# Kernel optimization log

Hardware: AMD Instinct MI355X
Metric: run time of the kernel (lower is better)

## Reference

```python
import jax, jax.numpy as jnp
import numpy as np
import math

# Dims chosen per input_specs
B, Q, S, T = 8, 64, 64, 64          # batch, queries, stat (segment) count, tokens per segment
H, DH = 8, 64                        # heads, head dim
NH = H * DH                          # num_hiddens = 512
STAT_K, TOKEN_K = 8, 16
NEG = -1e6


def setup_inputs() -> dict:
    key = jax.random.key(0)
    ks = jax.random.split(key, 11)
    f = lambda k, sh: jax.random.normal(k, sh, dtype=jnp.float32)
    w = lambda k: f(k, (NH, NH)) * 0.05  # Linear weights stored as [in, out]
    return {
        "queries": f(ks[0], (B, Q, NH)),
        "stat_keys": f(ks[1], (B, S, NH)),
        "token_keys": f(ks[2], (B * S, T, NH)),
        "values": f(ks[3], (B * S, T, NH)),
        "stat_valid_lens": jax.random.randint(ks[4], (B,), 1, S + 1, dtype=jnp.int32),
        "Wq_stat": w(ks[5]),
        "Wq_token": w(ks[6]),
        "Wk_stat": w(ks[7]),
        "Wk_token": w(ks[8]),
        "Wv": w(ks[9]),
        "Wo": w(ks[10]),
    }


def reference(queries, stat_keys, token_keys, values, stat_valid_lens,
              Wq_stat, Wq_token, Wk_stat, Wk_token, Wv, Wo):
    scale = 1.0 / math.sqrt(DH)

    def split_heads(x):  # [b, L, H*DH] -> [b, H, L, DH]
        b, L, _ = x.shape
        return x.reshape(b, L, H, DH).transpose(0, 2, 1, 3)

    q_stat = split_heads(queries @ Wq_stat)        # [B,H,Q,DH]
    q_tok = split_heads(queries @ Wq_token)        # [B,H,Q,DH]
    k_stat = split_heads(stat_keys @ Wk_stat)      # [B,H,S,DH]
    # token_keys/values come in as [B*S, T, size]; per-head layout [B,H,S,T,DH]
    k_tok = (token_keys @ Wk_token).reshape(B, S, T, H, DH).transpose(0, 3, 1, 2, 4)
    v = (values @ Wv).reshape(B, S, T, H, DH).transpose(0, 3, 1, 2, 4)

    # --- stat-level scores, valid-length mask, top-k sparsification, softmax ---
    stat_scores = jnp.einsum('bhqd,bhsd->bhqs', q_stat, k_stat) * scale  # [B,H,Q,S]
    valid = jnp.arange(S)[None, None, None, :] < stat_valid_lens[:, None, None, None]
    stat_scores = jnp.where(valid, stat_scores, NEG)
    k1 = min(S - 1, STAT_K)
    _, top_idx = jax.lax.top_k(stat_scores, k1)                           # [B,H,Q,k1]
    keep = jax.nn.one_hot(top_idx, S, dtype=stat_scores.dtype).sum(-2) > 0  # [B,H,Q,S]
    stat_w = jax.nn.softmax(jnp.where(keep, stat_scores, NEG), axis=-1)   # [B,H,Q,S]

    # --- token-level scores. NOTE: the original code computes torch.topk but then
    # overwrites with the LAST k2 positions (token_weights[:, :, -k2:] = ...), so the
    # token top-k result is dead code; we faithfully reproduce the last-k2 masking. ---
    tok_scores = jnp.einsum('bhqd,bhstd->bhsqt', q_tok, k_tok) * scale    # [B,H,S,Q,T]
    k2 = min(T - 1, TOKEN_K)
    last_mask = jnp.arange(T) >= (T - k2)
    tok_w = jax.nn.softmax(jnp.where(last_mask, tok_scores, NEG), axis=-1)
    tok_w = tok_w.transpose(0, 1, 3, 2, 4)                                # [B,H,Q,S,T]

    # --- combine hierarchy and attend over values ---
    comb = stat_w[..., None] * tok_w                                      # [B,H,Q,S,T]
    out = jnp.einsum('bhqst,bhstd->bhqd', comb, v)                        # [B,H,Q,DH]
    out = out.transpose(0, 2, 1, 3).reshape(B, Q, NH)
    return out @ Wo
```

## Files before the change

### kernel.cpp

```cpp
#include <hip/hip_runtime.h>
#include <hip/hip_bf16.h>

#define STAT_K 8
#define TOKEN_K 16

typedef short bf16x8 __attribute__((ext_vector_type(8)));
typedef float f32x4 __attribute__((ext_vector_type(4)));

__device__ inline ushort f2bf_rne(float x) {
    union { float f; unsigned u; } v; v.f = x;
    unsigned r = v.u + 0x7fff + ((v.u >> 16) & 1);
    return (ushort)(r >> 16);
}
__device__ inline float bf2f(ushort h) {
    union { unsigned u; float f; } v; v.u = ((unsigned)h) << 16;
    return v.f;
}

__global__ __launch_bounds__(256) void conv_w(
    const float* w0, const float* w1, const float* w2,
    const float* w3, const float* w4, const float* w5,
    ushort* wT)
{
    const int z = blockIdx.z;
    const float* srcs[6] = {w0, w1, w2, w3, w4, w5};
    const float* src = srcs[z];
    ushort* hi = wT + (size_t)z * 524288;
    ushort* lo = hi + 262144;
    __shared__ float t[32][33];
    const int c0 = blockIdx.x * 32, r0 = blockIdx.y * 32;
    const int tx = threadIdx.x & 31, ty = threadIdx.x >> 5;
    #pragma unroll
    for (int i = 0; i < 4; ++i)
        t[ty + 8 * i][tx] = src[(r0 + ty + 8 * i) * 512 + c0 + tx];
    __syncthreads();
    #pragma unroll
    for (int i = 0; i < 4; ++i) {
        float x = t[tx][ty + 8 * i];
        ushort h = f2bf_rne(x);
        int o = (c0 + ty + 8 * i) * 512 + r0 + tx;
        hi[o] = h;
        lo[o] = f2bf_rne(x - bf2f(h));
    }
}

__global__ __launch_bounds__(256) void gemm_all(
    const float* __restrict__ queries, const float* __restrict__ stat_keys,
    const float* __restrict__ token_keys, const float* __restrict__ values,
    const ushort* __restrict__ wT,
    float* __restrict__ q_stat, float* __restrict__ k_stat,
    float* __restrict__ q_tokf,
    ushort* __restrict__ k_tok, ushort* __restrict__ v_projT)
{
    __shared__ ushort smem[12800];
    const int tid = threadIdx.x;
    const int bid = blockIdx.x;
    const int wave = tid >> 6, lane = tid & 63;
    const int m16 = lane & 15, quad = lane >> 4;
    const int srow = tid >> 2, schunk = tid & 3;

    if (bid < 192) {
        const int z = bid >> 6, t = bid & 63;
        const int row0 = (t >> 3) * 64, col0 = (t & 7) * 64;
        const float* A = (z == 1) ? stat_keys : queries;
        const ushort* Bh = wT + (size_t)z * 524288;
        const ushort* Bl = Bh + 262144;
        float* C = (z == 0) ? q_stat : (z == 1) ? k_stat : q_tokf;

        ushort* As_hi = smem;
        ushort* As_lo = smem + 2560;
        ushort* Bs_hi = smem + 5120;
        ushort* Bs_lo = smem + 7680;
        const int wm = wave & 1, wn = wave >> 1;

        f32x4 acc[2][2];
        #pragma unroll
        for (int i = 0; i < 2; ++i)
            #pragma unroll
            for (int j = 0; j < 2; ++j)
                #pragma unroll
                for (int r = 0; r < 4; ++r) acc[i][j][r] = 0.f;

        for (int k0 = 0; k0 < 512; k0 += 32) {
            const float* ap = A + (size_t)(row0 + srow) * 512 + k0 + schunk * 8;
            float4 x0 = ((const float4*)ap)[0];
            float4 x1 = ((const float4*)ap)[1];
            ushort4 h0, l0, h1, l1;
            h0.x = f2bf_rne(x0.x); l0.x = f2bf_rne(x0.x - bf2f(h0.x));
            h0.y = f2bf_rne(x0.y); l0.y = f2bf_rne(x0.y - bf2f(h0.y));
            h0.z = f2bf_rne(x0.z); l0.z = f2bf_rne(x0.z - bf2f(h0.z));
            h0.w = f2bf_rne(x0.w); l0.w = f2bf_rne(x0.w - bf2f(h0.w));
            h1.x = f2bf_rne(x1.x); l1.x = f2bf_rne(x1.x - bf2f(h1.x));
            h1.y = f2bf_rne(x1.y); l1.y = f2bf_rne(x1.y - bf2f(h1.y));
            h1.z = f2bf_rne(x1.z); l1.z = f2bf_rne(x1.z - bf2f(h1.z));
            h1.w = f2bf_rne(x1.w); l1.w = f2bf_rne(x1.w - bf2f(h1.w));
            *(ushort4*)&As_hi[srow * 40 + schunk * 8]     = h0;
            *(ushort4*)&As_hi[srow * 40 + schunk * 8 + 4] = h1;
            *(ushort4*)&As_lo[srow * 40 + schunk * 8]     = l0;
            *(ushort4*)&As_lo[srow * 40 + schunk * 8 + 4] = l1;

            const size_t boff = (size_t)(col0 + srow) * 512 + k0 + schunk * 8;
            *(uint4*)&Bs_hi[srow * 40 + schunk * 8] = *(const uint4*)(Bh + boff);
            *(uint4*)&Bs_lo[srow * 40 + schunk * 8] = *(const uint4*)(Bl + boff);
            __syncthreads();

            bf16x8 af[2], bfv[2], afl[2], bfl[2];
            #pragma unroll
            for (int i = 0; i < 2; ++i) {
                af[i]  = *(const bf16x8*)&As_hi[(wm * 32 + i * 16 + m16) * 40 + quad * 8];
                bfv[i] = *(const bf16x8*)&Bs_hi[(wn * 32 + i * 16 + m16) * 40 + quad * 8];
                afl[i] = *(const bf16x8*)&As_lo[(wm * 32 + i * 16 + m16) * 40 + quad * 8];
                bfl[i] = *(const bf16x8*)&Bs_lo[(wn * 32 + i * 16 + m16) * 40 + quad * 8];
            }
            #pragma unroll
            for (int i = 0; i < 2; ++i)
                #pragma unroll
                for (int j = 0; j < 2; ++j) {
                    acc[i][j] = __builtin_amdgcn_mfma_f32_16x16x32_bf16(af[i],  bfv[j], acc[i][j], 0, 0, 0);
                    acc[i][j] = __builtin_amdgcn_mfma_f32_16x16x32_bf16(af[i],  bfl[j], acc[i][j], 0, 0, 0);
                    acc[i][j] = __builtin_amdgcn_mfma_f32_16x16x32_bf16(afl[i], bfv[j], acc[i][j], 0, 0, 0);
                }
            __syncthreads();
        }

        #pragma unroll
        for (int i = 0; i < 2; ++i)
            #pragma unroll
            for (int j = 0; j < 2; ++j) {
                int r0 = row0 + wm * 32 + i * 16 + quad * 4;
                int c = col0 + wn * 32 + j * 16 + m16;
                #pragma unroll
                for (int reg = 0; reg < 4; ++reg)
                    C[(size_t)(r0 + reg) * 512 + c] = acc[i][j][reg];
            }
    } else {
        const int u = bid - 192;
        const int z2 = u >> 8, vv = u & 255;
        const int col0 = (vv & 1) * 256, row0 = (vv >> 1) * 64;
        const float* A = z2 ? values : token_keys;
        const ushort* Bh = wT + (size_t)(z2 ? 4 : 3) * 524288;

        ushort* As = smem;
        ushort* Bs = smem + 2560;
        const int r = row0 + srow;
        const size_t arow = (size_t)((r >> 4) * 64 + 48 + (r & 15)) * 512;

        f32x4 acc[4][4];
        #pragma unroll
        for (int i = 0; i < 4; ++i)
            #pragma unroll
            for (int j = 0; j < 4; ++j)
                #pragma unroll
                for (int rr = 0; rr < 4; ++rr) acc[i][j][rr] = 0.f;

        for (int k0 = 0; k0 < 512; k0 += 32) {
            const float* ap = A + arow + k0 + schunk * 8;
            float4 x0 = ((const float4*)ap)[0];
            float4 x1 = ((const float4*)ap)[1];
            ushort4 h0, h1;
            h0.x = f2bf_rne(x0.x); h0.y = f2bf_rne(x0.y);
            h0.z = f2bf_rne(x0.z); h0.w = f2bf_rne(x0.w);
            h1.x = f2bf_rne(x1.x); h1.y = f2bf_rne(x1.y);
            h1.z = f2bf_rne(x1.z); h1.w = f2bf_rne(x1.w);
            *(ushort4*)&As[srow * 40 + schunk * 8]     = h0;
            *(ushort4*)&As[srow * 40 + schunk * 8 + 4] = h1;

            #pragma unroll
            for (int i = 0; i < 4; ++i) {
                int v = tid + i * 256;
                int brow = v >> 2, bchunk = v & 3;
                *(uint4*)&Bs[brow * 40 + bchunk * 8] =
                    *(const uint4*)(Bh + (size_t)(col0 + brow) * 512 + k0 + bchunk * 8);
            }
            __syncthreads();

            bf16x8 af[4], bf[4];
            #pragma unroll
            for (int i = 0; i < 4; ++i) {
                af[i] = *(const bf16x8*)&As[(i * 16 + m16) * 40 + quad * 8];
                bf[i] = *(const bf16x8*)&Bs[(wave * 64 + i * 16 + m16) * 40 + quad * 8];
            }
            #pragma unroll
            for (int i = 0; i < 4; ++i)
                #pragma unroll
                for (int j = 0; j < 4; ++j)
                    acc[i][j] = __builtin_amdgcn_mfma_f32_16x16x32_bf16(af[i], bf[j], acc[i][j], 0, 0, 0);
            __syncthreads();
        }

        #pragma unroll
        for (int i = 0; i < 4; ++i)
            #pragma unroll
            for (int j = 0; j < 4; ++j) {
                int rg = row0 + i * 16 + quad * 4;
                int c = col0 + wave * 64 + j * 16 + m16;
                if (z2 == 0) {
                    #pragma unroll
                    for (int reg = 0; reg < 4; ++reg)
                        k_tok[(size_t)(rg + reg) * 512 + c] = f2bf_rne(acc[i][j][reg]);
                } else {
                    int bb2 = rg >> 10, st = rg & 1023;
                    int hh = c >> 6, dd = c & 63;
                    ushort4 o4;
                    o4.x = f2bf_rne(acc[i][j][0]);
                    o4.y = f2bf_rne(acc[i][j][1]);
                    o4.z = f2bf_rne(acc[i][j][2]);
                    o4.w = f2bf_rne(acc[i][j][3]);
                    *(ushort4*)(v_projT + (((size_t)((bb2 * 8 + hh) * 64 + dd)) << 10) + st) = o4;
                }
            }
    }
}

__global__ __launch_bounds__(256) void fused_attend(
    const float* __restrict__ q_tokf, const float* __restrict__ q_stat,
    const float* __restrict__ k_stat, const int* __restrict__ valid_lens,
    const ushort* __restrict__ k_tok, const ushort* __restrict__ v_projT,
    ushort* __restrict__ ctx_hi, ushort* __restrict__ ctx_lo)
{
    const int bid = blockIdx.x;
    const int bh = bid >> 2, qb = bid & 3;
    const int b = bh >> 3, h = bh & 7;
    const int tid = threadIdx.x, wave = tid >> 6, lane = tid & 63;
    const int l15 = lane & 15, g = lane >> 4;
    const int q0 = qb * 16;

    __shared__ float  ks[64][68];
    __shared__ float  qsf[16][68];
    __shared__ ushort qs_hi[16][72], qs_lo[16][72];
    __shared__ float  sw[16][65];
    __shared__ ushort comb_hi[16][264], comb_lo[16][264];

    {
        const int qq = tid >> 4, c = (tid & 15) * 4;
        float4 x = *(const float4*)(q_tokf + (size_t)(b * 64 + q0 + qq) * 512 + h * 64 + c);
        ushort4 hx, lx;
        hx.x = f2bf_rne(x.x); lx.x = f2bf_rne(x.x - bf2f(hx.x));
        hx.y = f2bf_rne(x.y); lx.y = f2bf_rne(x.y - bf2f(hx.y));
        hx.z = f2bf_rne(x.z); lx.z = f2bf_rne(x.z - bf2f(hx.z));
        hx.w = f2bf_rne(x.w); lx.w = f2bf_rne(x.w - bf2f(hx.w));
        *(ushort4*)&qs_hi[qq][c] = hx;
        *(ushort4*)&qs_lo[qq][c] = lx;
        *(float4*)&qsf[qq][c] =
            *(const float4*)(q_stat + (size_t)(b * 64 + q0 + qq) * 512 + h * 64 + c);
        const int s = tid >> 2, c0 = (tid & 3) * 16;
        const float* kp = k_stat + (size_t)(b * 64 + s) * 512 + h * 64 + c0;
        #pragma unroll
        for (int i = 0; i < 4; ++i)
            *(float4*)&ks[s][c0 + 4 * i] = *(const float4*)(kp + 4 * i);
    }
    const int valid = valid_lens[b];
    __syncthreads();

    #pragma unroll
    for (int qi = 0; qi < 4; ++qi) {
        const int qq = wave * 4 + qi;
        const float4* kr = (const float4*)&ks[lane][0];
        const float4* qr = (const float4*)&qsf[qq][0];
        float sc = 0.f;
        #pragma unroll
        for (int i = 0; i < 16; ++i) {
            float4 a = qr[i], kk = kr[i];
            sc += a.x * kk.x + a.y * kk.y + a.z * kk.z + a.w * kk.w;
        }
        sc *= 0.125f;
        if (lane >= valid) sc = -1e6f;
        const float sc_keep = sc;
        float my = sc;
        bool picked = false;
        float m0 = 0.f, den = 0.f;
        #pragma unroll
        for (int j = 0; j < STAT_K; ++j) {
            float v = my;
            int idx = lane;
            #pragma unroll
            for (int off = 32; off > 0; off >>= 1) {
                float ov = __shfl_down(v, off);
                int   oi = __shfl_down(idx, off);
                if (ov > v || (ov == v && oi < idx)) { v = ov; idx = oi; }
            }
            v = __shfl(v, 0);
            idx = __shfl(idx, 0);
            if (j == 0) m0 = v;
            den += __expf(v - m0);
            if (lane == idx) { my = -3e38f; picked = true; }
        }
        sw[qq][lane] = picked ? __expf(sc_keep - m0) / den : 0.f;
    }
    __syncthreads();

    f32x4 accd;
    #pragma unroll
    for (int rr = 0; rr < 4; ++rr) accd[rr] = 0.f;

    const int swz = (l15 & 7) << 4;

    for (int ch = 0; ch < 4; ++ch) {
        const int sbase = ch * 16 + wave * 4;
        f32x4 sc[4];
        #pragma unroll
        for (int mt = 0; mt < 4; ++mt)
            #pragma unroll
            for (int rr = 0; rr < 4; ++rr) sc[mt][rr] = 0.f;

        #pragma unroll
        for (int ks2 = 0; ks2 < 2; ++ks2) {
            bf16x8 bhf = *(const bf16x8*)&qs_hi[l15][ks2 * 32 + g * 8];
            bf16x8 blf = *(const bf16x8*)&qs_lo[l15][ks2 * 32 + g * 8];
            #pragma unroll
            for (int mt = 0; mt < 4; ++mt) {
                const ushort* kp = k_tok +
                    (size_t)(b * 1024 + (sbase + mt) * 16 + l15) * 512 + h * 64 + ks2 * 32 + g * 8;
                bf16x8 a = *(const bf16x8*)kp;
                sc[mt] = __builtin_amdgcn_mfma_f32_16x16x32_bf16(a, bhf, sc[mt], 0, 0, 0);
                sc[mt] = __builtin_amdgcn_mfma_f32_16x16x32_bf16(a, blf, sc[mt], 0, 0, 0);
            }
        }

        #pragma unroll
        for (int mt = 0; mt < 4; ++mt) {
            float e0 = __expf(sc[mt][0] * 0.125f);
            float e1 = __expf(sc[mt][1] * 0.125f);
            float e2 = __expf(sc[mt][2] * 0.125f);
            float e3 = __expf(sc[mt][3] * 0.125f);
            float den = e0 + e1 + e2 + e3;
            den += __shfl_xor(den, 16);
            den += __shfl_xor(den, 32);
            float scl = sw[l15][sbase + mt] / den;
            ushort4 hx, lx;
            float c0 = e0 * scl; hx.x = f2bf_rne(c0); lx.x = f2bf_rne(c0 - bf2f(hx.x));
            float c1 = e1 * scl; hx.y = f2bf_rne(c1); lx.y = f2bf_rne(c1 - bf2f(hx.y));
            float c2 = e2 * scl; hx.z = f2bf_rne(c2); lx.z = f2bf_rne(c2 - bf2f(hx.z));
            float c3 = e3 * scl; hx.w = f2bf_rne(c3); lx.w = f2bf_rne(c3 - bf2f(hx.w));
            int colb = (((wave * 4 + mt) * 16 + g * 4) * 2) ^ swz;
            *(ushort4*)((char*)&comb_hi[l15][0] + colb) = hx;
            *(ushort4*)((char*)&comb_lo[l15][0] + colb) = lx;
        }
        __syncthreads();

        #pragma unroll
        for (int ks2 = 0; ks2 < 8; ++ks2) {
            const ushort* vp = v_projT +
                ((size_t)(bh * 64 + wave * 16 + l15) << 10) + ch * 256 + ks2 * 32 + g * 8;
            bf16x8 a = *(const bf16x8*)vp;
            int colb = ((ks2 * 32 + g * 8) * 2) ^ swz;
            bf16x8 bhf = *(const bf16x8*)((const char*)&comb_hi[l15][0] + colb);
            bf16x8 blf = *(const bf16x8*)((const char*)&comb_lo[l15][0] + colb);
            accd = __builtin_amdgcn_mfma_f32_16x16x32_bf16(a, bhf, accd, 0, 0, 0);
            accd = __builtin_amdgcn_mfma_f32_16x16x32_bf16(a, blf, accd, 0, 0, 0);
        }
        __syncthreads();
    }

    {
        size_t o = (size_t)(b * 64 + q0 + l15) * 512 + h * 64 + wave * 16 + g * 4;
        ushort4 hx, lx;
        #pragma unroll
        for (int rr = 0; rr < 4; ++rr) {
            ushort hh2 = f2bf_rne(accd[rr]);
            ((ushort*)&hx)[rr] = hh2;
            ((ushort*)&lx)[rr] = f2bf_rne(accd[rr] - bf2f(hh2));
        }
        *(ushort4*)(ctx_hi + o) = hx;
        *(ushort4*)(ctx_lo + o) = lx;
    }
}

__global__ __launch_bounds__(256) void gemm_out(
    const ushort* __restrict__ Ah, const ushort* __restrict__ Al,
    const ushort* __restrict__ Bh, const ushort* __restrict__ Bl,
    float* __restrict__ C)
{
    __shared__ ushort As[2][64][40];
    __shared__ ushort Bs[2][64][40];
    const int tid = threadIdx.x;
    const int row0 = blockIdx.y * 64, col0 = blockIdx.x * 64;
    const int wave = tid >> 6, lane = tid & 63;
    const int wm = wave & 1, wn = wave >> 1;
    const int m16 = lane & 15, quad = lane >> 4;
    const int srow = tid >> 2, schunk = tid & 3;

    f32x4 acc[2][2];
    #pragma unroll
    for (int i = 0; i < 2; ++i)
        #pragma unroll
        for (int j = 0; j < 2; ++j)
            #pragma unroll
            for (int r = 0; r < 4; ++r) acc[i][j][r] = 0.f;

    for (int k0 = 0; k0 < 512; k0 += 32) {
        const size_t aoff = (size_t)(row0 + srow) * 512 + k0 + schunk * 8;
        const size_t boff = (size_t)(col0 + srow) * 512 + k0 + schunk * 8;
        *(uint4*)&As[0][srow][schunk * 8] = *(const uint4*)(Ah + aoff);
        *(uint4*)&Bs[0][srow][schunk * 8] = *(const uint4*)(Bh + boff);
        *(uint4*)&As[1][srow][schunk * 8] = *(const uint4*)(Al + aoff);
        *(uint4*)&Bs[1][srow][schunk * 8] = *(const uint4*)(Bl + boff);
        __syncthreads();

        bf16x8 af[2], bf[2], afl[2], bfl[2];
        #pragma unroll
        for (int i = 0; i < 2; ++i) {
            af[i]  = *(const bf16x8*)&As[0][wm * 32 + i * 16 + m16][quad * 8];
            bf[i]  = *(const bf16x8*)&Bs[0][wn * 32 + i * 16 + m16][quad * 8];
            afl[i] = *(const bf16x8*)&As[1][wm * 32 + i * 16 + m16][quad * 8];
            bfl[i] = *(const bf16x8*)&Bs[1][wn * 32 + i * 16 + m16][quad * 8];
        }
        #pragma unroll
        for (int i = 0; i < 2; ++i)
            #pragma unroll
            for (int j = 0; j < 2; ++j) {
                acc[i][j] = __builtin_amdgcn_mfma_f32_16x16x32_bf16(af[i], bf[j], acc[i][j], 0, 0, 0);
                acc[i][j] = __builtin_amdgcn_mfma_f32_16x16x32_bf16(af[i], bfl[j], acc[i][j], 0, 0, 0);
                acc[i][j] = __builtin_amdgcn_mfma_f32_16x16x32_bf16(afl[i], bf[j], acc[i][j], 0, 0, 0);
            }
        __syncthreads();
    }

    #pragma unroll
    for (int i = 0; i < 2; ++i)
        #pragma unroll
        for (int j = 0; j < 2; ++j) {
            int r0 = row0 + wm * 32 + i * 16 + quad * 4;
            int c = col0 + wn * 32 + j * 16 + m16;
            #pragma unroll
            for (int reg = 0; reg < 4; ++reg)
                C[(size_t)(r0 + reg) * 512 + c] = acc[i][j][reg];
        }
}

extern "C" void kernel_launch(void* const* d_in, const int* in_sizes, int n_in,
                              void* d_out, int out_size, void* d_ws, size_t ws_size,
                              hipStream_t stream) {
    const float* queries    = (const float*)d_in[0];
    const float* stat_keys  = (const float*)d_in[1];
    const float* token_keys = (const float*)d_in[2];
    const float* values     = (const float*)d_in[3];
    const int*   valid_lens = (const int*)d_in[4];
    const float* Wq_stat    = (const float*)d_in[5];
    const float* Wq_token   = (const float*)d_in[6];
    const float* Wk_stat    = (const float*)d_in[7];
    const float* Wk_token   = (const float*)d_in[8];
    const float* Wv         = (const float*)d_in[9];
    const float* Wo         = (const float*)d_in[10];

    char* w = (char*)d_ws;
    ushort* wT      = (ushort*)(w + 0);
    float*  q_stat  = (float*)(w + 6291456);
    float*  k_stat  = (float*)(w + 7340032);
    float*  q_tokf  = (float*)(w + 8388608);
    ushort* k_tok   = (ushort*)(w + 9437184);
    ushort* v_projT = (ushort*)(w + 17825792);
    ushort* ctx_hi  = (ushort*)(w + 26214400);
    ushort* ctx_lo  = ctx_hi + 262144;

    ushort* wo_h = wT + 5 * 524288, *wo_l = wo_h + 262144;

    conv_w<<<dim3(16, 16, 6), 256, 0, stream>>>(
        Wq_stat, Wk_stat, Wq_token, Wk_token, Wv, Wo, wT);

    gemm_all<<<704, 256, 0, stream>>>(
        queries, stat_keys, token_keys, values, wT,
        q_stat, k_stat, q_tokf, k_tok, v_projT);

    fused_attend<<<256, 256, 0, stream>>>(
        q_tokf, q_stat, k_stat, valid_lens, k_tok, v_projT, ctx_hi, ctx_lo);

    gemm_out<<<dim3(8, 8), 256, 0, stream>>>(
        ctx_hi, ctx_lo, wo_h, wo_l, (float*)d_out);
}
```

Measured before the change: 222.0 us.

## Split attention into stat top-k kernel and chunk-parallel token attend with partial sums

Moves the stat-level scoring and top-k into a separate kernel with one 64-thread block per (batch, head, query). The token attention is split across four segment chunks, giving 1024 blocks instead of 256, and each block writes fp32 partial contexts. The output GEMM sums the four partials and does the hi/lo bf16 split while loading A. This raises parallelism in the attend stage at the cost of an extra launch and more global traffic for the partials.

```diff
diff --git a/kernel.cpp b/kernel.cpp
--- a/kernel.cpp
+++ b/kernel.cpp
@@ -212,23 +212,70 @@
     }
 }
 
-__global__ __launch_bounds__(256) void fused_attend(
-    const float* __restrict__ q_tokf, const float* __restrict__ q_stat,
-    const float* __restrict__ k_stat, const int* __restrict__ valid_lens,
-    const ushort* __restrict__ k_tok, const ushort* __restrict__ v_projT,
-    ushort* __restrict__ ctx_hi, ushort* __restrict__ ctx_lo)
+__global__ __launch_bounds__(64) void stat_topk(
+    const float* __restrict__ q_stat, const float* __restrict__ k_stat,
+    const int* __restrict__ valid_lens,
+    float* __restrict__ stat_wd)
 {
     const int bid = blockIdx.x;
-    const int bh = bid >> 2, qb = bid & 3;
+    const int b = bid >> 9;
+    const int hq = bid & 511;
+    const int h = hq >> 6;
+    const int q = hq & 63;
+    const int lane = threadIdx.x;
+
+    __shared__ float sq[64];
+    sq[lane] = q_stat[(b * 64 + q) * 512 + h * 64 + lane];
+    __syncthreads();
+
+    const float4* kr = (const float4*)(k_stat + (b * 64 + lane) * 512 + h * 64);
+    const float4* sq4 = (const float4*)sq;
+    float sc = 0.f;
+    #pragma unroll
+    for (int i = 0; i < 16; ++i) {
+        float4 a = sq4[i], kk = kr[i];
+        sc += a.x * kk.x + a.y * kk.y + a.z * kk.z + a.w * kk.w;
+    }
+    sc *= 0.125f;
+    if (lane >= valid_lens[b]) sc = -1e6f;
+
+    const float sc_keep = sc;
+    float my = sc;
+    bool picked = false;
+    float m0 = 0.f, den = 0.f;
+    #pragma unroll
+    for (int j = 0; j < STAT_K; ++j) {
+        float v = my;
+        int idx = lane;
+        #pragma unroll
+        for (int off = 32; off > 0; off >>= 1) {
+            float ov = __shfl_down(v, off);
+            int   oi = __shfl_down(idx, off);
+            if (ov > v || (ov == v && oi < idx)) { v = ov; idx = oi; }
+        }
+        v = __shfl(v, 0);
+        idx = __shfl(idx, 0);
+        if (j == 0) m0 = v;
+        den += __expf(v - m0);
+        if (lane == idx) { my = -3e38f; picked = true; }
+    }
+    stat_wd[(size_t)bid * 64 + lane] = picked ? __expf(sc_keep - m0) / den : 0.f;
+}
+
+__global__ __launch_bounds__(256) void tok_attend(
+    const float* __restrict__ q_tokf, const ushort* __restrict__ k_tok,
+    const ushort* __restrict__ v_projT, const float* __restrict__ stat_wd,
+    float* __restrict__ part)
+{
+    const int bid = blockIdx.x;
+    const int ch = bid & 3, qb = (bid >> 2) & 3, bh = bid >> 4;
     const int b = bh >> 3, h = bh & 7;
     const int tid = threadIdx.x, wave = tid >> 6, lane = tid & 63;
     const int l15 = lane & 15, g = lane >> 4;
     const int q0 = qb * 16;
 
-    __shared__ float  ks[64][68];
-    __shared__ float  qsf[16][68];
     __shared__ ushort qs_hi[16][72], qs_lo[16][72];
-    __shared__ float  sw[16][65];
+    __shared__ float  sw16[16][17];
     __shared__ ushort comb_hi[16][264], comb_lo[16][264];
 
     {
@@ -241,51 +288,52 @@
         hx.w = f2bf_rne(x.w); lx.w = f2bf_rne(x.w - bf2f(hx.w));
         *(ushort4*)&qs_hi[qq][c] = hx;
         *(ushort4*)&qs_lo[qq][c] = lx;
-        *(float4*)&qsf[qq][c] =
-            *(const float4*)(q_stat + (size_t)(b * 64 + q0 + qq) * 512 + h * 64 + c);
-        const int s = tid >> 2, c0 = (tid & 3) * 16;
-        const float* kp = k_stat + (size_t)(b * 64 + s) * 512 + h * 64 + c0;
-        #pragma unroll
-        for (int i = 0; i < 4; ++i)
-            *(float4*)&ks[s][c0 + 4 * i] = *(const float4*)(kp + 4 * i);
-    }
-    const int valid = valid_lens[b];
+        sw16[tid >> 4][tid & 15] =
+            stat_wd[(size_t)bh * 4096 + (q0 + (tid >> 4)) * 64 + ch * 16 + (tid & 15)];
+    }
     __syncthreads();
 
-    #pragma unroll
-    for (int qi = 0; qi < 4; ++qi) {
-        const int qq = wave * 4 + qi;
-        const float4* kr = (const float4*)&ks[lane][0];
-        const float4* qr = (const float4*)&qsf[qq][0];
-        float sc = 0.f;
-        #pragma unroll
-        for (int i = 0; i < 16; ++i) {
-            float4 a = qr[i], kk = kr[i];
-            sc += a.x * kk.x + a.y * kk.y + a.z * kk.z + a.w * kk.w;
-        }
-        sc *= 0.125f;
-        if (lane >= valid) sc = -1e6f;
-        const float sc_keep = sc;
-        float my = sc;
-        bool picked = false;
-        float m0 = 0.f, den = 0.f;
-        #pragma unroll
-        for (int j = 0; j < STAT_K; ++j) {
-            float v = my;
-            int idx = lane;
-            #pragma unroll
-            for (int off = 32; off > 0; off >>= 1) {
-                float ov = __shfl_down(v, off);
-                int   oi = __shfl_down(idx, off);
-                if (ov > v || (ov == v && oi < idx)) { v = ov; idx = oi; }
-            }
-            v = __shfl(v, 0);
-            idx = __shfl(idx, 0);
-            if (j == 0) m0 = v;
-            den += __expf(v - m0);
-            if (lane == idx) { my = -3e38f; picked = true; }
-        }
-        sw[qq][lane] = picked ? __expf(sc_keep - m0) / den : 0.f;
+    const int swz = (l15 & 7) << 4;
+
+    const int sbase = ch * 16 + wave * 4;
+    f32x4 sc[4];
+    #pragma unroll
+    for (int mt = 0; mt < 4; ++mt)
+        #pragma unroll
+        for (int rr = 0; rr < 4; ++rr) sc[mt][rr] = 0.f;
+
+    #pragma unroll
+    for (int ks2 = 0; ks2 < 2; ++ks2) {
+        bf16x8 bhf = *(const bf16x8*)&qs_hi[l15][ks2 * 32 + g * 8];
+        bf16x8 blf = *(const bf16x8*)&qs_lo[l15][ks2 * 32 + g * 8];
+        #pragma unroll
+        for (int mt = 0; mt < 4; ++mt) {
+            const ushort* kp = k_tok +
+                (size_t)(b * 1024 + (sbase + mt) * 16 + l15) * 512 + h * 64 + ks2 * 32 + g * 8;
+            bf16x8 a = *(const bf16x8*)kp;
+            sc[mt] = __builtin_amdgcn_mfma_f32_16x16x32_bf16(a, bhf, sc[mt], 0, 0, 0);
+            sc[mt] = __builtin_amdgcn_mfma_f32_16x16x32_bf16(a, blf, sc[mt], 0, 0, 0);
+        }
+    }
+
+    #pragma unroll
+    for (int mt = 0; mt < 4; ++mt) {
+        float e0 = __expf(sc[mt][0] * 0.125f);
+        float e1 = __expf(sc[mt][1] * 0.125f);
+        float e2 = __expf(sc[mt][2] * 0.125f);
+        float e3 = __expf(sc[mt][3] * 0.125f);
+        float den = e0 + e1 + e2 + e3;
+        den += __shfl_xor(den, 16);
+        den += __shfl_xor(den, 32);
+        float scl = sw16[l15][wave * 4 + mt] / den;
+        ushort4 hx, lx;
+        float c0 = e0 * scl; hx.x = f2bf_rne(c0); lx.x = f2bf_rne(c0 - bf2f(hx.x));
+        float c1 = e1 * scl; hx.y = f2bf_rne(c1); lx.y = f2bf_rne(c1 - bf2f(hx.y));
+        float c2 = e2 * scl; hx.z = f2bf_rne(c2); lx.z = f2bf_rne(c2 - bf2f(hx.z));
+        float c3 = e3 * scl; hx.w = f2bf_rne(c3); lx.w = f2bf_rne(c3 - bf2f(hx.w));
+        int colb = (((wave * 4 + mt) * 16 + g * 4) * 2) ^ swz;
+        *(ushort4*)((char*)&comb_hi[l15][0] + colb) = hx;
+        *(ushort4*)((char*)&comb_lo[l15][0] + colb) = lx;
     }
     __syncthreads();
 
@@ -293,81 +341,24 @@
     #pragma unroll
     for (int rr = 0; rr < 4; ++rr) accd[rr] = 0.f;
 
-    const int swz = (l15 & 7) << 4;
-
-    for (int ch = 0; ch < 4; ++ch) {
-        const int sbase = ch * 16 + wave * 4;
-        f32x4 sc[4];
-        #pragma unroll
-        for (int mt = 0; mt < 4; ++mt)
-            #pragma unroll
-            for (int rr = 0; rr < 4; ++rr) sc[mt][rr] = 0.f;
-
-        #pragma unroll
-        for (int ks2 = 0; ks2 < 2; ++ks2) {
-            bf16x8 bhf = *(const bf16x8*)&qs_hi[l15][ks2 * 32 + g * 8];
-            bf16x8 blf = *(const bf16x8*)&qs_lo[l15][ks2 * 32 + g * 8];
-            #pragma unroll
-            for (int mt = 0; mt < 4; ++mt) {
-                const ushort* kp = k_tok +
-                    (size_t)(b * 1024 + (sbase + mt) * 16 + l15) * 512 + h * 64 + ks2 * 32 + g * 8;
-                bf16x8 a = *(const bf16x8*)kp;
-                sc[mt] = __builtin_amdgcn_mfma_f32_16x16x32_bf16(a, bhf, sc[mt], 0, 0, 0);
-                sc[mt] = __builtin_amdgcn_mfma_f32_16x16x32_bf16(a, blf, sc[mt], 0, 0, 0);
-            }
-        }
-
-        #pragma unroll
-        for (int mt = 0; mt < 4; ++mt) {
-            float e0 = __expf(sc[mt][0] * 0.125f);
-            float e1 = __expf(sc[mt][1] * 0.125f);
-            float e2 = __expf(sc[mt][2] * 0.125f);
-            float e3 = __expf(sc[mt][3] * 0.125f);
-            float den = e0 + e1 + e2 + e3;
-            den += __shfl_xor(den, 16);
-            den += __shfl_xor(den, 32);
-            float scl = sw[l15][sbase + mt] / den;
-            ushort4 hx, lx;
-            float c0 = e0 * scl; hx.x = f2bf_rne(c0); lx.x = f2bf_rne(c0 - bf2f(hx.x));
-            float c1 = e1 * scl; hx.y = f2bf_rne(c1); lx.y = f2bf_rne(c1 - bf2f(hx.y));
-            float c2 = e2 * scl; hx.z = f2bf_rne(c2); lx.z = f2bf_rne(c2 - bf2f(hx.z));
-            float c3 = e3 * scl; hx.w = f2bf_rne(c3); lx.w = f2bf_rne(c3 - bf2f(hx.w));
-            int colb = (((wave * 4 + mt) * 16 + g * 4) * 2) ^ swz;
-            *(ushort4*)((char*)&comb_hi[l15][0] + colb) = hx;
-            *(ushort4*)((char*)&comb_lo[l15][0] + colb) = lx;
-        }
-        __syncthreads();
-
-        #pragma unroll
-        for (int ks2 = 0; ks2 < 8; ++ks2) {
-            const ushort* vp = v_projT +
-                ((size_t)(bh * 64 + wave * 16 + l15) << 10) + ch * 256 + ks2 * 32 + g * 8;
-            bf16x8 a = *(const bf16x8*)vp;
-            int colb = ((ks2 * 32 + g * 8) * 2) ^ swz;
-            bf16x8 bhf = *(const bf16x8*)((const char*)&comb_hi[l15][0] + colb);
-            bf16x8 blf = *(const bf16x8*)((const char*)&comb_lo[l15][0] + colb);
-            accd = __builtin_amdgcn_mfma_f32_16x16x32_bf16(a, bhf, accd, 0, 0, 0);
-            accd = __builtin_amdgcn_mfma_f32_16x16x32_bf16(a, blf, accd, 0, 0, 0);
-        }
-        __syncthreads();
-    }
-
-    {
-        size_t o = (size_t)(b * 64 + q0 + l15) * 512 + h * 64 + wave * 16 + g * 4;
-        ushort4 hx, lx;
-        #pragma unroll
-        for (int rr = 0; rr < 4; ++rr) {
-            ushort hh2 = f2bf_rne(accd[rr]);
-            ((ushort*)&hx)[rr] = hh2;
-            ((ushort*)&lx)[rr] = f2bf_rne(accd[rr] - bf2f(hh2));
-        }
-        *(ushort4*)(ctx_hi + o) = hx;
-        *(ushort4*)(ctx_lo + o) = lx;
-    }
+    #pragma unroll
+    for (int ks2 = 0; ks2 < 8; ++ks2) {
+        const ushort* vp = v_projT +
+            ((size_t)(bh * 64 + wave * 16 + l15) << 10) + ch * 256 + ks2 * 32 + g * 8;
+        bf16x8 a = *(const bf16x8*)vp;
+        int colb = ((ks2 * 32 + g * 8) * 2) ^ swz;
+        bf16x8 bhf = *(const bf16x8*)((const char*)&comb_hi[l15][0] + colb);
+        bf16x8 blf = *(const bf16x8*)((const char*)&comb_lo[l15][0] + colb);
+        accd = __builtin_amdgcn_mfma_f32_16x16x32_bf16(a, bhf, accd, 0, 0, 0);
+        accd = __builtin_amdgcn_mfma_f32_16x16x32_bf16(a, blf, accd, 0, 0, 0);
+    }
+
+    *(f32x4*)(part + ((size_t)(ch * 512 + b * 64 + q0 + l15) * 512)
+                    + h * 64 + wave * 16 + g * 4) = accd;
 }
 
 __global__ __launch_bounds__(256) void gemm_out(
-    const ushort* __restrict__ Ah, const ushort* __restrict__ Al,
+    const float* __restrict__ part,
     const ushort* __restrict__ Bh, const ushort* __restrict__ Bl,
     float* __restrict__ C)
 {
@@ -389,11 +380,30 @@
             for (int r = 0; r < 4; ++r) acc[i][j][r] = 0.f;
 
     for (int k0 = 0; k0 < 512; k0 += 32) {
-        const size_t aoff = (size_t)(row0 + srow) * 512 + k0 + schunk * 8;
+        const float* pb = part + (size_t)(row0 + srow) * 512 + k0 + schunk * 8;
+        float s[8];
+        #pragma unroll
+        for (int e = 0; e < 8; ++e) s[e] = 0.f;
+        #pragma unroll
+        for (int c = 0; c < 4; ++c) {
+            const float4* p4 = (const float4*)(pb + (size_t)c * 262144);
+            float4 a0 = p4[0], a1 = p4[1];
+            s[0] += a0.x; s[1] += a0.y; s[2] += a0.z; s[3] += a0.w;
+            s[4] += a1.x; s[5] += a1.y; s[6] += a1.z; s[7] += a1.w;
+        }
+        ushort hv[8], lv[8];
+        #pragma unroll
+        for (int e = 0; e < 8; ++e) {
+            hv[e] = f2bf_rne(s[e]);
+            lv[e] = f2bf_rne(s[e] - bf2f(hv[e]));
+        }
+        *(ushort4*)&As[0][srow][schunk * 8]     = *(ushort4*)&hv[0];
+        *(ushort4*)&As[0][srow][schunk * 8 + 4] = *(ushort4*)&hv[4];
+        *(ushort4*)&As[1][srow][schunk * 8]     = *(ushort4*)&lv[0];
+        *(ushort4*)&As[1][srow][schunk * 8 + 4] = *(ushort4*)&lv[4];
+
         const size_t boff = (size_t)(col0 + srow) * 512 + k0 + schunk * 8;
-        *(uint4*)&As[0][srow][schunk * 8] = *(const uint4*)(Ah + aoff);
         *(uint4*)&Bs[0][srow][schunk * 8] = *(const uint4*)(Bh + boff);
-        *(uint4*)&As[1][srow][schunk * 8] = *(const uint4*)(Al + aoff);
         *(uint4*)&Bs[1][srow][schunk * 8] = *(const uint4*)(Bl + boff);
         __syncthreads();
 
@@ -450,8 +460,8 @@
     float*  q_tokf  = (float*)(w + 8388608);
     ushort* k_tok   = (ushort*)(w + 9437184);
     ushort* v_projT = (ushort*)(w + 17825792);
-    ushort* ctx_hi  = (ushort*)(w + 26214400);
-    ushort* ctx_lo  = ctx_hi + 262144;
+    float*  stat_wd = (float*)(w + 26214400);
+    float*  part    = (float*)(w + 27262976);
 
     ushort* wo_h = wT + 5 * 524288, *wo_l = wo_h + 262144;
 
@@ -462,9 +472,9 @@
         queries, stat_keys, token_keys, values, wT,
         q_stat, k_stat, q_tokf, k_tok, v_projT);
 
-    fused_attend<<<256, 256, 0, stream>>>(
-        q_tokf, q_stat, k_stat, valid_lens, k_tok, v_projT, ctx_hi, ctx_lo);
-
-    gemm_out<<<dim3(8, 8), 256, 0, stream>>>(
-        ctx_hi, ctx_lo, wo_h, wo_l, (float*)d_out);
-}
+    stat_topk<<<4096, 64, 0, stream>>>(q_stat, k_stat, valid_lens, stat_wd);
+
+    tok_attend<<<1024, 256, 0, stream>>>(q_tokf, k_tok, v_projT, stat_wd, part);
+
+    gemm_out<<<dim3(8, 8), 256, 0, stream>>>(part, wo_h, wo_l, (float*)d_out);
+}
```

Result: no change. 221.8 us (-0.1%).
